# Performance work log

Measured on AMD Instinct MI355X. Metric: run time of the kernel, lower is better.

The kernel has to match this reference:

```python
import jax, jax.numpy as jnp
import numpy as np

N_NODES = 100000
N_EDGES = 320000
N_GRAPHS = 4096
HID = 256
NUM_FEAT = 28


def setup_inputs() -> dict:
    key = jax.random.key(0)
    ks = jax.random.split(key, 20)
    inp = {}
    inp['x'] = jax.random.normal(ks[0], (N_NODES, NUM_FEAT), dtype=jnp.float32)
    inp['edge_index'] = jax.random.randint(ks[1], (2, N_EDGES), 0, N_NODES, dtype=jnp.int64)
    inp['batch'] = jnp.sort(jax.random.randint(ks[2], (N_NODES,), 0, N_GRAPHS, dtype=jnp.int64))
    def lin(k, out_d, in_d, scale=None):
        s = scale if scale is not None else 1.0 / np.sqrt(in_d)
        return jax.random.uniform(k, (out_d, in_d), jnp.float32, -s, s)
    # GraphConv layer l: W_rel (neighbor aggregate), b_rel, W_root (self)
    dims = [(HID, NUM_FEAT), (HID, HID), (HID, HID), (HID, HID)]
    for i, (o, d) in enumerate(dims, 1):
        inp[f'W{i}_rel'] = lin(ks[2 + 3 * i], o, d)
        inp[f'b{i}_rel'] = jnp.zeros((o,), jnp.float32)
        inp[f'W{i}_root'] = lin(ks[3 + 3 * i], o, d)
    inp['fc1_w'] = lin(ks[15], HID, 4 * HID)
    inp['fc1_b'] = jnp.zeros((HID,), jnp.float32)
    inp['fc2_w'] = lin(ks[16], HID, HID)
    inp['fc2_b'] = jnp.zeros((HID,), jnp.float32)
    inp['fc3_w'] = lin(ks[17], HID, HID)
    inp['fc3_b'] = jnp.zeros((HID,), jnp.float32)
    inp['fc4_w'] = lin(ks[18], 1, HID)
    inp['fc4_b'] = jnp.zeros((1,), jnp.float32)
    return inp


def _graph_conv(x, src, dst, W_rel, b_rel, W_root):
    # PyG GraphConv (aggr='add'): out = lin_rel(sum_{j->i} x_j) + lin_root(x_i)
    agg = jax.ops.segment_sum(x[src], dst, num_segments=N_NODES)  # [N, d]
    return agg @ W_rel.T + b_rel + x @ W_root.T


def reference(x, edge_index, batch,
              W1_rel, b1_rel, W1_root, W2_rel, b2_rel, W2_root,
              W3_rel, b3_rel, W3_root, W4_rel, b4_rel, W4_root,
              fc1_w, fc1_b, fc2_w, fc2_b, fc3_w, fc3_b, fc4_w, fc4_b):
    src, dst = edge_index[0], edge_index[1]
    x1 = jax.nn.relu(_graph_conv(x, src, dst, W1_rel, b1_rel, W1_root))
    x2 = jax.nn.relu(_graph_conv(x1, src, dst, W2_rel, b2_rel, W2_root))
    x3 = jax.nn.relu(_graph_conv(x2, src, dst, W3_rel, b3_rel, W3_root))
    x4 = jax.nn.relu(_graph_conv(x3, src, dst, W4_rel, b4_rel, W4_root))
    h = jnp.concatenate([x1, x2, x3, x4], axis=-1)  # [N, 4*HID]
    # global mean pool over graphs
    sums = jax.ops.segment_sum(h, batch, num_segments=N_GRAPHS)  # [G, 4*HID]
    cnts = jax.ops.segment_sum(jnp.ones((h.shape[0],), h.dtype), batch, num_segments=N_GRAPHS)
    g = sums / jnp.maximum(cnts, 1.0)[:, None]
    g = jax.nn.relu(g @ fc1_w.T + fc1_b)
    g = jax.nn.relu(g @ fc2_w.T + fc2_b)
    g = jax.nn.relu(g @ fc3_w.T + fc3_b)
    out = g @ fc4_w.T + fc4_b  # [G, 1]
    return out.reshape(-1)
```

## Files before the change

### kernel.cpp

```cpp
#include <hip/hip_runtime.h>
#include <hip/hip_bf16.h>
#include <cstdio>

#define HID 256

using short8  = __attribute__((ext_vector_type(8))) short;
using floatx4 = __attribute__((ext_vector_type(4))) float;

__device__ inline unsigned short bf16_rn(float x) {
    unsigned u = __float_as_uint(x);
    return (unsigned short)((u + 0x7FFFu + ((u >> 16) & 1u)) >> 16);
}

__global__ void marker_k(float* __restrict__ out, int n, float v) {
    int i = blockIdx.x * blockDim.x + threadIdx.x;
    if (i < n) out[i] = v;
}

__global__ void detect64_k(const unsigned* __restrict__ eiw, int E,
                           const unsigned* __restrict__ bw, int Nh,
                           int* __restrict__ any_nonzero) {
    int total = E + Nh;
    unsigned loc = 0;
    for (int i = blockIdx.x * blockDim.x + threadIdx.x; i < total;
         i += gridDim.x * blockDim.x) {
        loc |= (i < E) ? eiw[2 * i + 1] : bw[2 * (i - E) + 1];
    }
    if (loc) atomicOr(any_nonzero, 1);
}

__global__ void norm_idx_k(const int* __restrict__ src, int* __restrict__ dst,
                           int n, const int* __restrict__ any_nonzero) {
    int is64 = (any_nonzero[0] == 0);
    for (int i = blockIdx.x * blockDim.x + threadIdx.x; i < n;
         i += gridDim.x * blockDim.x) {
        dst[i] = is64 ? src[2 * i] : src[i];
    }
}

__global__ void pool_bounds_k(const int* __restrict__ batch, int N, int G,
                              int* __restrict__ starts) {
    int g = blockIdx.x * blockDim.x + threadIdx.x;
    if (g > G) return;
    int lo = 0, hi = N;
    while (lo < hi) {
        int mid = (lo + hi) >> 1;
        if (batch[mid] < g) lo = mid + 1; else hi = mid;
    }
    starts[g] = lo;
}

__global__ void deg_count_k(const int* __restrict__ ei, int E, int N,
                            int* __restrict__ deg) {
    int e = blockIdx.x * blockDim.x + threadIdx.x;
    if (e >= E) return;
    int s = ei[e];
    int d = ei[E + e];
    if ((unsigned)s >= (unsigned)N || (unsigned)d >= (unsigned)N) return;
    atomicAdd(&deg[d], 1);
}

#define SCAN_BLK 256

__global__ __launch_bounds__(SCAN_BLK) void scan_a_k(const int* __restrict__ deg,
                                                     int* __restrict__ bsum, int N) {
    __shared__ int red[SCAN_BLK];
    int i = blockIdx.x * SCAN_BLK + threadIdx.x;
    int v = (i < N) ? deg[i] : 0;
    red[threadIdx.x] = v;
    __syncthreads();
#pragma unroll
    for (int off = SCAN_BLK / 2; off > 0; off >>= 1) {
        if (threadIdx.x < off) red[threadIdx.x] += red[threadIdx.x + off];
        __syncthreads();
    }
    if (threadIdx.x == 0) bsum[blockIdx.x] = red[0];
}

__global__ __launch_bounds__(1024) void scan_b_k(int* __restrict__ bsum, int nb) {
    __shared__ int tsum[1024];
    int t = threadIdx.x;
    int v = (t < nb) ? bsum[t] : 0;
    tsum[t] = v;
    __syncthreads();
    for (int off = 1; off < 1024; off <<= 1) {
        int u = (t >= off) ? tsum[t - off] : 0;
        __syncthreads();
        tsum[t] += u;
        __syncthreads();
    }
    if (t < nb) bsum[t] = tsum[t] - v;
}

__global__ __launch_bounds__(SCAN_BLK) void scan_c_k(const int* __restrict__ deg,
                                                     const int* __restrict__ bsum,
                                                     int* __restrict__ row_ptr, int N) {
    __shared__ int tsum[SCAN_BLK];
    int t = threadIdx.x;
    int i = blockIdx.x * SCAN_BLK + t;
    int v = (i < N) ? deg[i] : 0;
    tsum[t] = v;
    __syncthreads();
    for (int off = 1; off < SCAN_BLK; off <<= 1) {
        int u = (t >= off) ? tsum[t - off] : 0;
        __syncthreads();
        tsum[t] += u;
        __syncthreads();
    }
    if (i <= N) row_ptr[i] = tsum[t] - v + bsum[blockIdx.x];
}

__global__ __launch_bounds__(1024) void scan_rowptr_k(const int* __restrict__ deg,
                                                      int* __restrict__ row_ptr, int N) {
    __shared__ int tsum[1024];
    int t = threadIdx.x;
    int chunk = (N + 1023) / 1024;
    int lo = t * chunk;
    int hi = min(lo + chunk, N);
    int s = 0;
    for (int i = lo; i < hi; i++) s += deg[i];
    tsum[t] = s;
    __syncthreads();
    for (int off = 1; off < 1024; off <<= 1) {
        int v = (t >= off) ? tsum[t - off] : 0;
        __syncthreads();
        tsum[t] += v;
        __syncthreads();
    }
    int run = (t == 0) ? 0 : tsum[t - 1];
    for (int i = lo; i < hi; i++) { row_ptr[i] = run; run += deg[i]; }
    if (hi >= N && lo <= N) row_ptr[N] = run;
}

__global__ void fill_csr_k(const int* __restrict__ ei, int E, int N,
                           const int* __restrict__ row_ptr, int* __restrict__ cursor,
                           int* __restrict__ esrc) {
    int e = blockIdx.x * blockDim.x + threadIdx.x;
    if (e >= E) return;
    int s = ei[e];
    int d = ei[E + e];
    if ((unsigned)s >= (unsigned)N || (unsigned)d >= (unsigned)N) return;
    int pos = atomicAdd(&cursor[d], 1);
    esrc[row_ptr[d] + pos] = s;
}

__global__ void gather28_k(const float* __restrict__ x, const int* __restrict__ row_ptr,
                           const int* __restrict__ esrc, float* __restrict__ Q28, int N) {
    int gid = blockIdx.x * blockDim.x + threadIdx.x;
    int node = gid >> 5;
    if (node >= N) return;
    int lane = gid & 31;
    if (lane >= 28) return;
    int s = row_ptr[node], e = row_ptr[node + 1];
    float acc = 0.f;
    for (int i = s; i < e; i++) {
        int src = esrc[i];
        acc += x[(size_t)src * 28 + lane];
    }
    Q28[(size_t)node * 28 + lane] = acc;
}

__global__ void gather256_k(const float* __restrict__ P, const int* __restrict__ row_ptr,
                            const int* __restrict__ esrc, float* __restrict__ Q, int N) {
    int gid = blockIdx.x * blockDim.x + threadIdx.x;
    int node = gid >> 6;
    if (node >= N) return;
    int lane = gid & 63;
    int s = row_ptr[node], e = row_ptr[node + 1];
    float4 acc = make_float4(0.f, 0.f, 0.f, 0.f);
    for (int i = s; i < e; i++) {
        int src = esrc[i];
        float4 v = *(const float4*)(P + (size_t)src * HID + lane * 4);
        acc.x += v.x; acc.y += v.y; acc.z += v.z; acc.w += v.w;
    }
    *(float4*)(Q + (size_t)node * HID + lane * 4) = acc;
}

__global__ __launch_bounds__(256) void l1_fused_k(
    const float* __restrict__ x, const float* __restrict__ agg,
    const float* __restrict__ Wrel, const float* __restrict__ Wroot,
    const float* __restrict__ bias, float* __restrict__ out, int M) {
    __shared__ float As[64][28];
    __shared__ float Xs[64][28];
    int t = threadIdx.x;
    int n0 = blockIdx.x * 64;
    float wrel[28], wroot[28];
#pragma unroll
    for (int k = 0; k < 28; k++) {
        wrel[k]  = Wrel[t * 28 + k];
        wroot[k] = Wroot[t * 28 + k];
    }
    float b = bias[t];
    for (int idx = t; idx < 64 * 28; idx += 256) {
        int r = idx / 28;
        int c = idx - r * 28;
        int gr = n0 + r;
        As[r][c] = (gr < M) ? agg[(size_t)gr * 28 + c] : 0.f;
        Xs[r][c] = (gr < M) ? x[(size_t)gr * 28 + c] : 0.f;
    }
    __syncthreads();
    int nmax = min(64, M - n0);
    for (int n = 0; n < nmax; n++) {
        float acc = b;
#pragma unroll
        for (int k4 = 0; k4 < 28; k4 += 4) {
            float4 a  = *(const float4*)&As[n][k4];
            float4 xx = *(const float4*)&Xs[n][k4];
            acc += a.x * wrel[k4] + a.y * wrel[k4 + 1] + a.z * wrel[k4 + 2] + a.w * wrel[k4 + 3];
            acc += xx.x * wroot[k4] + xx.y * wroot[k4 + 1] + xx.z * wroot[k4 + 2] + xx.w * wroot[k4 + 3];
        }
        out[(size_t)(n0 + n) * HID + t] = fmaxf(acc, 0.f);
    }
}

__global__ void wsplit6_k(const float* W0, const float* W1, const float* W2,
                          const float* W3, const float* W4, const float* W5,
                          unsigned short* __restrict__ out_hl, int n) {
    int i = blockIdx.x * blockDim.x + threadIdx.x;
    if (i >= n) return;
    const float* W = (blockIdx.y == 0) ? W0 : (blockIdx.y == 1) ? W1 :
                     (blockIdx.y == 2) ? W2 : (blockIdx.y == 3) ? W3 :
                     (blockIdx.y == 4) ? W4 : W5;
    unsigned short* o = out_hl + (size_t)blockIdx.y * 2 * n;
    float a = W[i];
    unsigned short h = bf16_rn(a);
    float hf = __uint_as_float(((unsigned)h) << 16);
    o[i] = h;
    o[n + i] = bf16_rn(a - hf);
}

#define LSTR 40

__global__ __launch_bounds__(256) void gemm_strip_mfma_k(
    const float* __restrict__ Q, const unsigned short* __restrict__ Wr_hl,
    float* __restrict__ P, const unsigned short* __restrict__ Wo_hl,
    const float* __restrict__ bias, int M) {
    __shared__ unsigned short Ah[64 * LSTR], Al[64 * LSTR];
    __shared__ unsigned short Wh[256 * LSTR], Wl[256 * LSTR];
    int t = threadIdx.x;
    int brow = blockIdx.x * 64;
    int w = t >> 6;
    int l = t & 63;

    floatx4 acc[4][4];
#pragma unroll
    for (int i = 0; i < 4; i++)
#pragma unroll
        for (int j = 0; j < 4; j++) acc[i][j] = (floatx4){0.f, 0.f, 0.f, 0.f};

    int srow = t >> 2;
    int sg   = t & 3;

    for (int ch = 0; ch < 16; ch++) {
        int phase2 = (ch >= 8);
        const float* A = phase2 ? P : Q;
        const unsigned short* Whl = phase2 ? Wo_hl : Wr_hl;
        int kbase = (ch & 7) * 32;

        {
            int gr = brow + srow;
            float v[8];
            if (gr < M) {
                float4 u0 = *(const float4*)(A + (size_t)gr * HID + kbase + sg * 8);
                float4 u1 = *(const float4*)(A + (size_t)gr * HID + kbase + sg * 8 + 4);
                v[0] = u0.x; v[1] = u0.y; v[2] = u0.z; v[3] = u0.w;
                v[4] = u1.x; v[5] = u1.y; v[6] = u1.z; v[7] = u1.w;
            } else {
#pragma unroll
                for (int j = 0; j < 8; j++) v[j] = 0.f;
            }
            union { unsigned short us[8]; short8 v8; } hh, ll;
#pragma unroll
            for (int j = 0; j < 8; j++) {
                unsigned short h = bf16_rn(v[j]);
                float hf = __uint_as_float(((unsigned)h) << 16);
                hh.us[j] = h;
                ll.us[j] = bf16_rn(v[j] - hf);
            }
            int base = srow * LSTR + sg * 8;
            *(short8*)(Ah + base) = hh.v8;
            *(short8*)(Al + base) = ll.v8;
        }
#pragma unroll
        for (int i = 0; i < 4; i++) {
            int col = srow + i * 64;
            short8 hh = *(const short8*)(Whl + (size_t)col * HID + kbase + sg * 8);
            short8 ll = *(const short8*)(Whl + 65536 + (size_t)col * HID + kbase + sg * 8);
            int base = col * LSTR + sg * 8;
            *(short8*)(Wh + base) = hh;
            *(short8*)(Wl + base) = ll;
        }
        __syncthreads();

        int frow = l & 15;
        int fg   = l >> 4;
        short8 ahf[4], alf[4], whf[4], wlf[4];
#pragma unroll
        for (int rt = 0; rt < 4; rt++) {
            int base = (rt * 16 + frow) * LSTR + fg * 8;
            ahf[rt] = *(short8*)(Ah + base);
            alf[rt] = *(short8*)(Al + base);
        }
#pragma unroll
        for (int ct = 0; ct < 4; ct++) {
            int base = (w * 64 + ct * 16 + frow) * LSTR + fg * 8;
            whf[ct] = *(short8*)(Wh + base);
            wlf[ct] = *(short8*)(Wl + base);
        }
#pragma unroll
        for (int rt = 0; rt < 4; rt++)
#pragma unroll
            for (int ct = 0; ct < 4; ct++) {
                acc[rt][ct] = __builtin_amdgcn_mfma_f32_16x16x32_bf16(
                    ahf[rt], whf[ct], acc[rt][ct], 0, 0, 0);
                acc[rt][ct] = __builtin_amdgcn_mfma_f32_16x16x32_bf16(
                    alf[rt], whf[ct], acc[rt][ct], 0, 0, 0);
                acc[rt][ct] = __builtin_amdgcn_mfma_f32_16x16x32_bf16(
                    ahf[rt], wlf[ct], acc[rt][ct], 0, 0, 0);
            }
        __syncthreads();
    }

#pragma unroll
    for (int ct = 0; ct < 4; ct++) {
        int gc = w * 64 + ct * 16 + (l & 15);
        float bs = bias[gc];
#pragma unroll
        for (int rt = 0; rt < 4; rt++) {
            floatx4 a = acc[rt][ct];
#pragma unroll
            for (int r = 0; r < 4; r++) {
                int gr = brow + rt * 16 + (l >> 4) * 4 + r;
                if (gr < M)
                    P[(size_t)gr * HID + gc] = fmaxf(a[r] + bs, 0.f);
            }
        }
    }
}

__global__ __launch_bounds__(256) void pool_slice_k(const float* __restrict__ xl,
                                                    const int* __restrict__ starts,
                                                    float* __restrict__ gslice, int N) {
    int g = blockIdx.x;
    int t = threadIdx.x;
    int s = starts[g], e = starts[g + 1];
    s = max(0, min(s, N));
    e = max(s, min(e, N));
    float a = 0.f;
    for (int n = s; n < e; n++) a += xl[(size_t)n * HID + t];
    float inv = 1.f / (float)max(e - s, 1);
    gslice[(size_t)g * 1024 + t] = a * inv;
}

#define BM 64
#define BN 64
#define BK 32
#define LP 68

__global__ __launch_bounds__(256) void gemm_dual_k(
    const float* __restrict__ A1, int lda1, const float* __restrict__ W1,
    const float* __restrict__ A2, int lda2, const float* __restrict__ W2,
    const float* __restrict__ bias, float* __restrict__ out, int ldout,
    int M, int K1, int K2, int relu) {
    __shared__ float As[BK][LP];
    __shared__ float Ws[BK][LP];
    int t = threadIdx.x;
    int brow = blockIdx.x * BM;
    int bcol = blockIdx.y * BN;
    int tx = t & 15, ty = t >> 4;
    float acc[4][4] = {{0.f}};
    int Ktot = K1 + K2;
    int srow = t >> 3;
    int sk4 = (t & 7) << 2;

    for (int kk = 0; kk < Ktot; kk += BK) {
        int phase2 = (kk >= K1);
        const float* A = phase2 ? A2 : A1;
        const float* W = phase2 ? W2 : W1;
        int lda = phase2 ? lda2 : lda1;
        int ldw = phase2 ? K2 : K1;
        int kbase = phase2 ? (kk - K1) : kk;
#pragma unroll
        for (int i = 0; i < 2; i++) {
            int r = srow + i * 32;
            int gr = brow + r;
            float4 v = make_float4(0.f, 0.f, 0.f, 0.f);
            if (gr < M) v = *(const float4*)(A + (size_t)gr * lda + kbase + sk4);
            As[sk4 + 0][r] = v.x; As[sk4 + 1][r] = v.y;
            As[sk4 + 2][r] = v.z; As[sk4 + 3][r] = v.w;
            float4 w = *(const float4*)(W + (size_t)(bcol + r) * ldw + kbase + sk4);
            Ws[sk4 + 0][r] = w.x; Ws[sk4 + 1][r] = w.y;
            Ws[sk4 + 2][r] = w.z; Ws[sk4 + 3][r] = w.w;
        }
        __syncthreads();
#pragma unroll
        for (int k = 0; k < BK; k++) {
            float4 a = *(const float4*)&As[k][ty << 2];
            float4 w = *(const float4*)&Ws[k][tx << 2];
            float av[4] = {a.x, a.y, a.z, a.w};
            float wv[4] = {w.x, w.y, w.z, w.w};
#pragma unroll
            for (int i = 0; i < 4; i++)
#pragma unroll
                for (int j = 0; j < 4; j++)
                    acc[i][j] = fmaf(av[i], wv[j], acc[i][j]);
        }
        __syncthreads();
    }
#pragma unroll
    for (int i = 0; i < 4; i++) {
        int gr = brow + (ty << 2) + i;
        if (gr >= M) continue;
#pragma unroll
        for (int j = 0; j < 4; j++) {
            int gc = bcol + (tx << 2) + j;
            float v = acc[i][j] + bias[gc];
            if (relu) v = fmaxf(v, 0.f);
            out[(size_t)gr * ldout + gc] = v;
        }
    }
}

__global__ void fc4_k(const float* __restrict__ in, const float* __restrict__ w,
                      const float* __restrict__ b, float* __restrict__ out, int M) {
    int gid = blockIdx.x * blockDim.x + threadIdx.x;
    int row = gid >> 6;
    if (row >= M) return;
    int lane = gid & 63;
    float4 v  = *(const float4*)(in + (size_t)row * HID + lane * 4);
    float4 ww = *(const float4*)(w + lane * 4);
    float acc = v.x * ww.x + v.y * ww.y + v.z * ww.z + v.w * ww.w;
#pragma unroll
    for (int off = 32; off; off >>= 1) acc += __shfl_down(acc, off);
    if (lane == 0) out[row] = acc + b[0];
}

extern "C" void kernel_launch(void* const* d_in, const int* in_sizes, int n_in,
                              void* d_out, int out_size, void* d_ws, size_t ws_size,
                              hipStream_t stream) {
    const int N = in_sizes[0] / 28;
    const int E = in_sizes[1] / 2;
    const int G = out_size;

    const float* x        = (const float*)d_in[0];
    const int*   ei_raw   = (const int*)d_in[1];
    const int*   b_raw    = (const int*)d_in[2];
    const float* W1_rel  = (const float*)d_in[3];
    const float* b1      = (const float*)d_in[4];
    const float* W1_root = (const float*)d_in[5];
    const float* W2_rel  = (const float*)d_in[6];
    const float* b2      = (const float*)d_in[7];
    const float* W2_root = (const float*)d_in[8];
    const float* W3_rel  = (const float*)d_in[9];
    const float* b3      = (const float*)d_in[10];
    const float* W3_root = (const float*)d_in[11];
    const float* W4_rel  = (const float*)d_in[12];
    const float* b4      = (const float*)d_in[13];
    const float* W4_root = (const float*)d_in[14];
    const float* fc1_w = (const float*)d_in[15];
    const float* fc1_b = (const float*)d_in[16];
    const float* fc2_w = (const float*)d_in[17];
    const float* fc2_b = (const float*)d_in[18];
    const float* fc3_w = (const float*)d_in[19];
    const float* fc3_b = (const float*)d_in[20];
    const float* fc4_w = (const float*)d_in[21];
    const float* fc4_b = (const float*)d_in[22];
    float* out = (float*)d_out;

    size_t fN  = (size_t)N * HID;
    size_t off_P      = 0;
    size_t off_Q      = off_P + fN;
    size_t off_gpool  = off_Q + fN;
    size_t off_t1     = off_gpool + (size_t)G * 1024;
    size_t off_t2     = off_t1 + (size_t)G * HID;
    size_t off_ei     = off_t2 + (size_t)G * HID;
    size_t off_batch  = off_ei + (size_t)2 * E;
    size_t off_starts = off_batch + (size_t)N;
    size_t off_flag   = off_starts + (size_t)(G + 1);
    size_t off_deg    = off_flag + 1;
    size_t off_cur    = off_deg + (size_t)N;
    size_t off_rowp   = off_cur + (size_t)N;
    size_t off_bsum   = off_rowp + (size_t)(N + 1);
    size_t off_esrc   = off_bsum + 1024;
    size_t off_wsplit = off_esrc + (size_t)E;
    size_t need = (off_wsplit + 393216 + 16) * 4;

    if (ws_size < need) {
        fprintf(stderr, "[kernel_launch] ws too small: ws=%zu need=%zu\n", ws_size, need);
        marker_k<<<(G + 255) / 256, 256, 0, stream>>>(out, G, (float)(ws_size >> 20));
        return;
    }

    float* wsf   = (float*)d_ws;
    float* P     = wsf + off_P;
    float* Q     = wsf + off_Q;
    float* gpool = wsf + off_gpool;
    float* t1    = wsf + off_t1;
    float* t2    = wsf + off_t2;
    int* nei     = (int*)(wsf + off_ei);
    int* nbatch  = (int*)(wsf + off_batch);
    int* starts  = (int*)(wsf + off_starts);
    int* flag    = (int*)(wsf + off_flag);
    int* deg     = (int*)(wsf + off_deg);
    int* cursor  = (int*)(wsf + off_cur);
    int* row_ptr = (int*)(wsf + off_rowp);
    int* bsum    = (int*)(wsf + off_bsum);
    int* esrc    = (int*)(wsf + off_esrc);
    unsigned short* wsplit = (unsigned short*)(wsf + off_wsplit);

    hipMemsetAsync(flag, 0, sizeof(int), stream);
    detect64_k<<<1024, 256, 0, stream>>>((const unsigned*)ei_raw, E,
                                         (const unsigned*)b_raw, N / 2, flag);
    norm_idx_k<<<1024, 256, 0, stream>>>(ei_raw, nei, 2 * E, flag);
    norm_idx_k<<<512, 256, 0, stream>>>(b_raw, nbatch, N, flag);

    pool_bounds_k<<<(G + 1 + 255) / 256, 256, 0, stream>>>(nbatch, N, G, starts);

    hipMemsetAsync(deg, 0, 2 * (size_t)N * sizeof(int), stream);
    deg_count_k<<<(E + 255) / 256, 256, 0, stream>>>(nei, E, N, deg);
    int nb = (N + 1 + SCAN_BLK - 1) / SCAN_BLK;
    if (nb <= 1024) {
        scan_a_k<<<nb, SCAN_BLK, 0, stream>>>(deg, bsum, N);
        scan_b_k<<<1, 1024, 0, stream>>>(bsum, nb);
        scan_c_k<<<nb, SCAN_BLK, 0, stream>>>(deg, bsum, row_ptr, N);
    } else {
        scan_rowptr_k<<<1, 1024, 0, stream>>>(deg, row_ptr, N);
    }
    fill_csr_k<<<(E + 255) / 256, 256, 0, stream>>>(nei, E, N, row_ptr, cursor, esrc);

    wsplit6_k<<<dim3((65536 + 255) / 256, 6), 256, 0, stream>>>(
        W2_rel, W2_root, W3_rel, W3_root, W4_rel, W4_root, wsplit, 65536);

    int nstrips = (N + 63) / 64;

    gather28_k<<<((size_t)N * 32 + 255) / 256, 256, 0, stream>>>(x, row_ptr, esrc, Q, N);
    l1_fused_k<<<nstrips, 256, 0, stream>>>(x, Q, W1_rel, W1_root, b1, P, N);
    pool_slice_k<<<G, 256, 0, stream>>>(P, starts, gpool + 0, N);

    const float* bb[3] = {b2, b3, b4};
    for (int l = 0; l < 3; l++) {
        gather256_k<<<((size_t)N * 64 + 255) / 256, 256, 0, stream>>>(P, row_ptr, esrc, Q, N);
        gemm_strip_mfma_k<<<nstrips, 256, 0, stream>>>(
            Q, wsplit + (size_t)(2 * l) * 131072,
            P, wsplit + (size_t)(2 * l + 1) * 131072, bb[l], N);
        pool_slice_k<<<G, 256, 0, stream>>>(P, starts, gpool + 256 * (l + 1), N);
    }

    dim3 gdimG(G / BM, HID / BN);
    gemm_dual_k<<<gdimG, 256, 0, stream>>>(gpool, 1024, fc1_w, nullptr, 0, nullptr,
                                           fc1_b, t1, HID, G, 1024, 0, 1);
    gemm_dual_k<<<gdimG, 256, 0, stream>>>(t1, HID, fc2_w, nullptr, 0, nullptr,
                                           fc2_b, t2, HID, G, HID, 0, 1);
    gemm_dual_k<<<gdimG, 256, 0, stream>>>(t2, HID, fc3_w, nullptr, 0, nullptr,
                                           fc3_b, t1, HID, G, HID, 0, 1);
    fc4_k<<<(G * 64 + 255) / 256, 256, 0, stream>>>(t1, fc4_w, fc4_b, out, G);
}
```

Before: 1.030 ms.

## Pre-swizzle split weights and load them into LDS with global_load_lds

The weight-split kernel now writes the bf16 hi/lo weights in a per-K-chunk, XOR-swizzled layout that matches the LDS tile the GEMM reads. The GEMM then copies each weight chunk straight from global memory into LDS with the direct global-to-LDS load builtin, instead of staging it through registers into a padded array. This removes the register round-trip and VGPR use for the weight tiles and shrinks weight LDS from padded to dense, with the swizzle meant to avoid bank conflicts. It relies on exact layout agreement between the producer and consumer, and on alignment of the workspace offset, which is now rounded up.

```diff
diff --git a/kernel.cpp b/kernel.cpp
--- a/kernel.cpp
+++ b/kernel.cpp
@@ -7,9 +7,15 @@
 using short8  = __attribute__((ext_vector_type(8))) short;
 using floatx4 = __attribute__((ext_vector_type(4))) float;
 
+typedef const unsigned int __attribute__((address_space(1)))* as1_cuintp;
+typedef unsigned int __attribute__((address_space(3)))* as3_uintp;
+
 __device__ inline unsigned short bf16_rn(float x) {
     unsigned u = __float_as_uint(x);
     return (unsigned short)((u + 0x7FFFu + ((u >> 16) & 1u)) >> 16);
+}
+__device__ inline float bf2f(unsigned short u) {
+    return __uint_as_float(((unsigned)u) << 16);
 }
 
 __global__ void marker_k(float* __restrict__ out, int n, float v) {
@@ -221,12 +227,19 @@
     const float* W = (blockIdx.y == 0) ? W0 : (blockIdx.y == 1) ? W1 :
                      (blockIdx.y == 2) ? W2 : (blockIdx.y == 3) ? W3 :
                      (blockIdx.y == 4) ? W4 : W5;
-    unsigned short* o = out_hl + (size_t)blockIdx.y * 2 * n;
+    unsigned short* o = out_hl + (size_t)blockIdx.y * 131072;
     float a = W[i];
     unsigned short h = bf16_rn(a);
-    float hf = __uint_as_float(((unsigned)h) << 16);
-    o[i] = h;
-    o[n + i] = bf16_rn(a - hf);
+    unsigned short lo = bf16_rn(a - bf2f(h));
+    int col = i >> 8;
+    int k   = i & 255;
+    int ch  = k >> 5;
+    int sg  = (k >> 3) & 3;
+    int e   = k & 7;
+    int gp  = sg ^ ((col >> 1) & 3);
+    size_t base = (size_t)ch * 16384 + (size_t)col * 32 + gp * 8 + e;
+    o[base] = h;
+    o[base + 8192] = lo;
 }
 
 #define LSTR 40
@@ -236,7 +249,7 @@
     float* __restrict__ P, const unsigned short* __restrict__ Wo_hl,
     const float* __restrict__ bias, int M) {
     __shared__ unsigned short Ah[64 * LSTR], Al[64 * LSTR];
-    __shared__ unsigned short Wh[256 * LSTR], Wl[256 * LSTR];
+    __shared__ unsigned short Wlin[16384];
     int t = threadIdx.x;
     int brow = blockIdx.x * 64;
     int w = t >> 6;
@@ -281,14 +294,16 @@
             *(short8*)(Ah + base) = hh.v8;
             *(short8*)(Al + base) = ll.v8;
         }
-#pragma unroll
-        for (int i = 0; i < 4; i++) {
-            int col = srow + i * 64;
-            short8 hh = *(const short8*)(Whl + (size_t)col * HID + kbase + sg * 8);
-            short8 ll = *(const short8*)(Whl + 65536 + (size_t)col * HID + kbase + sg * 8);
-            int base = col * LSTR + sg * 8;
-            *(short8*)(Wh + base) = hh;
-            *(short8*)(Wl + base) = ll;
+        {
+            const char* wg = (const char*)(Whl + (size_t)(ch & 7) * 16384);
+#pragma unroll
+            for (int i = 0; i < 8; i++) {
+                int boff = w * 8192 + i * 1024;
+                __builtin_amdgcn_global_load_lds(
+                    (as1_cuintp)(const void*)(wg + boff + l * 16),
+                    (as3_uintp)(void*)((char*)Wlin + boff),
+                    16, 0, 0);
+            }
         }
         __syncthreads();
 
@@ -303,9 +318,11 @@
         }
 #pragma unroll
         for (int ct = 0; ct < 4; ct++) {
-            int base = (w * 64 + ct * 16 + frow) * LSTR + fg * 8;
-            whf[ct] = *(short8*)(Wh + base);
-            wlf[ct] = *(short8*)(Wl + base);
+            int col = w * 64 + ct * 16 + frow;
+            int gp = fg ^ ((col >> 1) & 3);
+            int base = col * 32 + gp * 8;
+            whf[ct] = *(short8*)(Wlin + base);
+            wlf[ct] = *(short8*)(Wlin + 8192 + base);
         }
 #pragma unroll
         for (int rt = 0; rt < 4; rt++)
@@ -482,7 +499,7 @@
     size_t off_rowp   = off_cur + (size_t)N;
     size_t off_bsum   = off_rowp + (size_t)(N + 1);
     size_t off_esrc   = off_bsum + 1024;
-    size_t off_wsplit = off_esrc + (size_t)E;
+    size_t off_wsplit = (off_esrc + (size_t)E + 3) & ~(size_t)3;
     size_t need = (off_wsplit + 393216 + 16) * 4;
 
     if (ws_size < need) {
```

After: 984.4 us. -4.4%, faster.
